# Optimization experiments

Hardware: AMD Instinct MI355X
Metric: run time of the kernel (lower is better)

## Reference

```python
import jax, jax.numpy as jnp
import numpy as np

N, E, C_IN, HID, K, NLAYERS = 1024, 2048, 4, 192, 5, 4


def setup_inputs() -> dict:
    key = jax.random.key(0)
    ks = jax.random.split(key, 24)
    s = 0.05
    x = jax.random.normal(ks[0], (N, C_IN), jnp.float32)
    src = jax.random.randint(ks[1], (E,), 0, N, dtype=jnp.int32)
    off = jax.random.randint(ks[2], (E,), 1, N, dtype=jnp.int32)
    dst = (src + off) % N  # guarantees no self-loops (ChebConv removes them)
    edge_index = jnp.stack([src, dst])  # [2, E] int32
    edge_attr = jax.random.normal(ks[3], (E, C_IN), jnp.float32)
    batch = jnp.zeros((N,), jnp.int32)  # unused by forward, kept for signature fidelity
    inp = {
        'x': x, 'edge_index': edge_index, 'edge_attr': edge_attr, 'batch': batch,
        # ChebConv(4, 192, K=5): K weight mats + bias
        'cheb_w': jax.random.normal(ks[4], (K, C_IN, HID), jnp.float32) * s,
        'cheb_b': jnp.zeros((HID,), jnp.float32),
        # edge encoder Linear(4, 192)
        'eenc_w': jax.random.normal(ks[5], (C_IN, HID), jnp.float32) * s,
        'eenc_b': jnp.zeros((HID,), jnp.float32),
        # 4 NNConv layers, each with MapE2NxN edge MLP (192->192->192*192),
        # root linear (192x192, no bias) and conv bias
        'nn1_w': jax.random.normal(ks[6], (NLAYERS, HID, HID), jnp.float32) * s,
        'nn1_b': jnp.zeros((NLAYERS, HID), jnp.float32),
        'nn2_w': jax.random.normal(ks[7], (NLAYERS, HID, HID * HID), jnp.float32) * (s / 8.0),
        'nn2_b': jnp.zeros((NLAYERS, HID * HID), jnp.float32),
        'root_w': jax.random.normal(ks[8], (NLAYERS, HID, HID), jnp.float32) * s,
        'conv_b': jnp.zeros((NLAYERS, HID), jnp.float32),
        # LayerNorm per DeepGCNLayer
        'ln_g': jnp.ones((NLAYERS, HID), jnp.float32),
        'ln_b': jnp.zeros((NLAYERS, HID), jnp.float32),
        # final Linear(192, 2)
        'out_w': jax.random.normal(ks[9], (HID, 2), jnp.float32) * s,
        'out_b': jnp.zeros((2,), jnp.float32),
    }
    return inp


def _layernorm(v, g, b):
    mu = jnp.mean(v, axis=-1, keepdims=True)
    var = jnp.mean(jnp.square(v - mu), axis=-1, keepdims=True)
    return (v - mu) * jax.lax.rsqrt(var + 1e-5) * g + b


def reference(x, edge_index, edge_attr, batch, cheb_w, cheb_b, eenc_w, eenc_b,
              nn1_w, nn1_b, nn2_w, nn2_b, root_w, conv_b, ln_g, ln_b, out_w, out_b):
    n = x.shape[0]
    src, dst = edge_index[0], edge_index[1]

    # ---- ChebConv (sym norm, lambda_max=2.0) => L_hat = -D^{-1/2} A D^{-1/2} ----
    deg = jax.ops.segment_sum(jnp.ones_like(src, dtype=x.dtype), src, num_segments=n)
    dinv = jnp.where(deg > 0, 1.0 / jnp.sqrt(jnp.maximum(deg, 1.0)), 0.0)
    wnorm = -dinv[src] * dinv[dst]  # [E]

    def lap(v):  # y = L_hat @ v : gather -> weight -> scatter-add
        return jax.ops.segment_sum(wnorm[:, None] * v[src], dst, num_segments=n)

    Tx0 = x
    out = Tx0 @ cheb_w[0]
    Tx1 = lap(Tx0)
    out = out + Tx1 @ cheb_w[1]
    for k in range(2, K):  # Chebyshev recurrence
        Tx2 = 2.0 * lap(Tx1) - Tx0
        out = out + Tx2 @ cheb_w[k]
        Tx0, Tx1 = Tx1, Tx2
    h = out + cheb_b  # [N, HID]

    # ---- edge encoder ----
    ea = edge_attr @ eenc_w + eenc_b  # [E, HID]

    # ---- NNConv: per-edge MLP-generated weight, gather->edge-GEMM->scatter ----
    def nnconv(v, i):
        theta = (ea @ nn1_w[i] + nn1_b[i]) @ nn2_w[i] + nn2_b[i]  # [E, HID*HID]
        theta = theta.reshape(E, HID, HID)
        msg = jnp.einsum('ei,eio->eo', v[src], theta)  # per-edge matvec
        agg = jax.ops.segment_sum(msg, dst, num_segments=n)  # aggr='add'
        return agg + v @ root_w[i] + conv_b[i]

    # layers[0].conv applied directly (no pre-norm/act)
    h = nnconv(h, 0)
    # layers[1:4] are DeepGCNLayer res+: x + conv(dropout(act(norm(x))))
    for i in range(1, NLAYERS):
        z = jax.nn.relu(_layernorm(h, ln_g[i], ln_b[i]))
        h = h + nnconv(z, i)
    # final: act(layers[0].norm(x)), dropout (eval=identity), linear
    h = jax.nn.relu(_layernorm(h, ln_g[0], ln_b[0]))
    return h @ out_w + out_b  # [N, 2]
```

## Files before the change

kernel.cpp:

```cpp
#include <hip/hip_runtime.h>
#include <stdint.h>

typedef _Float16 half8 __attribute__((ext_vector_type(8)));
typedef float f32x4 __attribute__((ext_vector_type(4)));

typedef const __attribute__((address_space(1))) void* gptr_t;
typedef __attribute__((address_space(3))) void* lptr_t;
static __device__ __forceinline__ void gll16(const void* g, void* l) {
  __builtin_amdgcn_global_load_lds((gptr_t)(unsigned long long)g,
                                   (lptr_t)(unsigned int)(unsigned long long)l,
                                   16, 0, 0);
}

__global__ __launch_bounds__(256)
void k_pb(const float* __restrict__ nn2_w, const float* __restrict__ nn2_b,
          const float* __restrict__ eenc_w, const float* __restrict__ eenc_b,
          const float* __restrict__ nn1_w, const float* __restrict__ nn1_b,
          const float* __restrict__ root_w, _Float16* __restrict__ Btl,
          const float* __restrict__ x, const int* __restrict__ ei,
          float* __restrict__ Tx, int* __restrict__ rowptr, int* __restrict__ eord) {
  __shared__ __align__(16) float smem[17344];
  int t = threadIdx.x;
  if (blockIdx.x >= 72) {
    if (blockIdx.x == 72) {
      if (blockIdx.y == 0) {
        float* cur = smem;
        float* yv = smem + 4096;
        float* deg = yv;
        for (int i = t; i < 1024; i += 256) deg[i] = 0.f;
        __syncthreads();
        for (int e = t; e < 2048; e += 256) atomicAdd(&deg[ei[e]], 1.f);
        __syncthreads();
        float wn[8];
#pragma unroll
        for (int i = 0; i < 8; ++i) {
          int e = t + 256 * i;
          int s = ei[e], d = ei[2048 + e];
          float ds = deg[s], dd = deg[d];
          float a = ds > 0.f ? 1.f / sqrtf(fmaxf(ds, 1.f)) : 0.f;
          float bb = dd > 0.f ? 1.f / sqrtf(fmaxf(dd, 1.f)) : 0.f;
          wn[i] = -a * bb;
        }
        __syncthreads();
        float4 prev[4];
#pragma unroll
        for (int q = 0; q < 4; ++q) {
          int i = t + 256 * q;
          float4 xv = ((const float4*)x)[i];
          ((float4*)cur)[i] = xv;
          ((float4*)Tx)[i] = xv;
        }
        __syncthreads();
        for (int rec = 0; rec < 4; ++rec) {
          for (int i = t; i < 4096; i += 256) yv[i] = 0.f;
          __syncthreads();
#pragma unroll
          for (int i = 0; i < 8; ++i) {
            int e = t + 256 * i;
            int s = ei[e], d = ei[2048 + e];
            float wv = wn[i];
#pragma unroll
            for (int c = 0; c < 4; ++c) atomicAdd(&yv[d * 4 + c], wv * cur[s * 4 + c]);
          }
          __syncthreads();
          float a = rec ? 2.f : 1.f;
#pragma unroll
          for (int q = 0; q < 4; ++q) {
            int i = t + 256 * q;
            float4 y4 = ((float4*)yv)[i];
            float4 c4 = ((float4*)cur)[i];
            float4 n4;
            n4.x = a * y4.x - (rec ? prev[q].x : 0.f);
            n4.y = a * y4.y - (rec ? prev[q].y : 0.f);
            n4.z = a * y4.z - (rec ? prev[q].z : 0.f);
            n4.w = a * y4.w - (rec ? prev[q].w : 0.f);
            prev[q] = c4;
            ((float4*)cur)[i] = n4;
            ((float4*)(Tx + (rec + 1) * 4096))[i] = n4;
          }
          __syncthreads();
        }
      } else if (blockIdx.y == 1) {
        int* cnt = (int*)smem;
        int* rp  = (int*)smem + 1024;
        int* wtot = (int*)smem + 2048;
        int lane = t & 63, wv = t >> 6;
        for (int i = t; i < 1024; i += 256) cnt[i] = 0;
        __syncthreads();
        for (int e = t; e < 2048; e += 256) atomicAdd(&cnt[ei[2048 + e]], 1);
        __syncthreads();
        int c0 = cnt[t * 4], c1 = cnt[t * 4 + 1], c2 = cnt[t * 4 + 2], c3 = cnt[t * 4 + 3];
        int s = c0 + c1 + c2 + c3;
        int inc = s;
#pragma unroll
        for (int off = 1; off < 64; off <<= 1) {
          int u = __shfl_up(inc, off);
          if (lane >= off) inc += u;
        }
        if (lane == 63) wtot[wv] = inc;
        __syncthreads();
        int woff = 0;
#pragma unroll
        for (int j = 0; j < 4; ++j) if (j < wv) woff += wtot[j];
        int excl = woff + inc - s;
        int4 r4; r4.x = excl; r4.y = excl + c0; r4.z = excl + c0 + c1; r4.w = excl + c0 + c1 + c2;
        *(int4*)(rowptr + t * 4) = r4;
        if (t == 0) rowptr[1024] = 2048;
        rp[t * 4] = r4.x; rp[t * 4 + 1] = r4.y; rp[t * 4 + 2] = r4.z; rp[t * 4 + 3] = r4.w;
        __syncthreads();
        for (int e = t; e < 2048; e += 256) {
          int d = ei[2048 + e];
          int slot = atomicAdd(&rp[d], 1);
          eord[slot] = e;
        }
      }
      return;
    }
    int l = blockIdx.y;
    for (int idx = t; idx < 36864; idx += 256) {
      float v = root_w[(size_t)l * 36864 + idx];
      int i = idx / 192, o = idx - i * 192;
      Btl[(size_t)l * 221184 + (i >> 3) * 9216 + (size_t)(960 + o) * 8 + (i & 7)] = (_Float16)v;
    }
    return;
  }
  int w = t >> 6, lane = t & 63;
  int l = blockIdx.y;
  int wcol = blockIdx.x * 512 + w * 128;
  const float* W2l = nn2_w + (size_t)l * 7077888;
  char* ldsbase = (char*)smem + w * 16384;
  int rlane = lane >> 5;
  int clane = (lane & 31) << 4;
  float2 nb = *(const float2*)(nn2_b + (size_t)l * 36864 + wcol + 2 * lane);

#define ISSUE(tile)                                                             \
  {                                                                             \
    _Pragma("unroll")                                                           \
    for (int j = 0; j < 4; ++j) {                                               \
      int row = (tile) * 8 + 2 * j + rlane;                                     \
      gll16((const char*)(W2l + (size_t)row * 36864 + wcol) + clane,            \
            ldsbase + ((tile) & 3) * 4096 + j * 1024 + lane * 16);              \
    }                                                                           \
  }

  ISSUE(0); ISSUE(1); ISSUE(2);
  if (t < 192) {
    float a0 = 0.f, a1 = 0.f, a2 = 0.f, a3 = 0.f, a4 = 0.f;
    const float* nw = nn1_w + (size_t)l * 36864 + t;
    for (int k = 0; k < 192; ++k) {
      float nv = nw[(size_t)k * 192];
      a0 += eenc_w[k] * nv;
      a1 += eenc_w[192 + k] * nv;
      a2 += eenc_w[384 + k] * nv;
      a3 += eenc_w[576 + k] * nv;
      a4 += eenc_b[k] * nv;
    }
    smem[16384 + t] = a0; smem[16576 + t] = a1; smem[16768 + t] = a2;
    smem[16960 + t] = a3; smem[17152 + t] = a4 + nn1_b[l * 192 + t];
  }
  __syncthreads();

  float2 a0 = {0.f, 0.f}, a1 = {0.f, 0.f}, a2 = {0.f, 0.f}, a3 = {0.f, 0.f}, a4 = {0.f, 0.f};
  const float* Ms = smem + 16384;
  for (int tile = 0; tile < 24; ++tile) {
    if (tile < 21) ISSUE(tile + 3);
    if (tile < 21)       asm volatile("s_waitcnt vmcnt(12)" ::: "memory");
    else if (tile == 21) asm volatile("s_waitcnt vmcnt(8)" ::: "memory");
    else if (tile == 22) asm volatile("s_waitcnt vmcnt(4)" ::: "memory");
    else                 asm volatile("s_waitcnt vmcnt(0)" ::: "memory");
    const float* wb = smem + w * 4096 + (tile & 3) * 1024;
    const float* Mt = Ms + tile * 8;
#pragma unroll
    for (int r = 0; r < 8; ++r) {
      float2 wv = *(const float2*)(wb + r * 128 + 2 * lane);
      float m0 = Mt[r], m1 = Mt[192 + r], m2 = Mt[384 + r], m3 = Mt[576 + r], m4 = Mt[768 + r];
      a0.x += m0 * wv.x; a0.y += m0 * wv.y;
      a1.x += m1 * wv.x; a1.y += m1 * wv.y;
      a2.x += m2 * wv.x; a2.y += m2 * wv.y;
      a3.x += m3 * wv.x; a3.y += m3 * wv.y;
      a4.x += m4 * wv.x; a4.y += m4 * wv.y;
    }
  }
#undef ISSUE
  a4.x += nb.x; a4.y += nb.y;
  int col = wcol + 2 * lane;
  {
    int i0 = col / 192, o0 = col - i0 * 192;
    _Float16* B0 = Btl + (size_t)l * 221184 + (i0 >> 3) * 9216 + (i0 & 7);
    B0[(size_t)(0 * 192 + o0) * 8] = (_Float16)a0.x;
    B0[(size_t)(1 * 192 + o0) * 8] = (_Float16)a1.x;
    B0[(size_t)(2 * 192 + o0) * 8] = (_Float16)a2.x;
    B0[(size_t)(3 * 192 + o0) * 8] = (_Float16)a3.x;
    B0[(size_t)(4 * 192 + o0) * 8] = (_Float16)a4.x;
    int c1 = col + 1;
    int i1 = c1 / 192, o1 = c1 - i1 * 192;
    _Float16* B1 = Btl + (size_t)l * 221184 + (i1 >> 3) * 9216 + (i1 & 7);
    B1[(size_t)(0 * 192 + o1) * 8] = (_Float16)a0.y;
    B1[(size_t)(1 * 192 + o1) * 8] = (_Float16)a1.y;
    B1[(size_t)(2 * 192 + o1) * 8] = (_Float16)a2.y;
    B1[(size_t)(3 * 192 + o1) * 8] = (_Float16)a3.y;
    B1[(size_t)(4 * 192 + o1) * 8] = (_Float16)a4.y;
  }
}

__global__ __launch_bounds__(256)
void k_y(const _Float16* __restrict__ z16, const _Float16* __restrict__ Btl,
         float* __restrict__ Y, const float* __restrict__ Tx,
         const float* __restrict__ cheb_w, const float* __restrict__ cheb_b, int layer) {
  __shared__ __align__(16) _Float16 Als[12288];
  int t = threadIdx.x;
  int w = t >> 6, lane = t & 63, l15 = lane & 15, q4 = lane >> 4;
  int e0 = blockIdx.x * 64, cb = blockIdx.y;
  if (layer == 0) {
#pragma unroll
    for (int it = 0; it < 6; ++it) {
      int u = it * 256 + t;
      int row = u & 63, ck = u >> 6;
      int n = e0 + row;
      float tv[5][4];
#pragma unroll
      for (int k = 0; k < 5; ++k) {
        float4 t4 = ((const float4*)(Tx + k * 4096))[n];
        tv[k][0] = t4.x; tv[k][1] = t4.y; tv[k][2] = t4.z; tv[k][3] = t4.w;
      }
      union { _Float16 h[8]; uint4 v; } u8;
#pragma unroll
      for (int j = 0; j < 8; ++j) {
        int o = ck * 8 + j;
        float acc = cheb_b[o];
#pragma unroll
        for (int k = 0; k < 5; ++k)
#pragma unroll
          for (int c = 0; c < 4; ++c)
            acc += tv[k][c] * cheb_w[(k * 4 + c) * 192 + o];
        u8.h[j] = (_Float16)acc;
      }
      *(uint4*)(Als + (size_t)u * 8) = u8.v;
    }
    __syncthreads();
  }
  const _Float16* Bt = Btl + (size_t)layer * 221184;
  const _Float16* ap = z16 + (((size_t)q4 * 1024) + e0 + w * 16 + l15) * 8;
  const _Float16* bp = Bt + (((size_t)q4 * 1152) + cb * 192 + l15) * 8;
  f32x4 acc[12] = {};
#pragma unroll
  for (int ks = 0; ks < 6; ++ks) {
    half8 av;
    if (layer == 0)
      av = *(const half8*)(Als + (((size_t)(ks * 4 + q4) * 64) + w * 16 + l15) * 8);
    else
      av = *(const half8*)(ap + (size_t)ks * 4 * 1024 * 8);
#pragma unroll
    for (int nt = 0; nt < 12; ++nt) {
      half8 bv = *(const half8*)(bp + (size_t)ks * 4 * 1152 * 8 + nt * 16 * 8);
      acc[nt] = __builtin_amdgcn_mfma_f32_16x16x32_f16(av, bv, acc[nt], 0, 0, 0);
    }
  }
#pragma unroll
  for (int nt = 0; nt < 12; ++nt) {
    int col = cb * 192 + nt * 16 + l15;
#pragma unroll
    for (int r = 0; r < 4; ++r) {
      int row = e0 + w * 16 + q4 * 4 + r;
      Y[(size_t)row * 1152 + col] = acc[nt][r];
    }
  }
}

__global__ __launch_bounds__(256)
void k_gn(const int* __restrict__ ei, const float* __restrict__ eattr,
          const int* __restrict__ rowptr, const int* __restrict__ eord,
          const float* __restrict__ Y, const float* __restrict__ hp,
          const float* __restrict__ cbv, const float* __restrict__ gg,
          const float* __restrict__ bb, float* __restrict__ ho,
          _Float16* __restrict__ zo, const float* __restrict__ out_w,
          const float* __restrict__ out_b, float* __restrict__ outp, int l) {
  int t = threadIdx.x, w = t >> 6, lane = t & 63;
  int n = blockIdx.x * 4 + w;
  int o0 = lane, o1 = lane + 64, o2 = lane + 128;
  float v0 = 0.f, v1 = 0.f, v2 = 0.f;
  int beg = rowptr[n], end = rowptr[n + 1];
  for (int idx = beg; idx < end; ++idx) {
    int e = eord[idx];
    int s = ei[e];
    float4 u = ((const float4*)eattr)[e];
    const float* yr = Y + (size_t)s * 1152;
    v0 += yr[o0] * u.x + yr[192 + o0] * u.y + yr[384 + o0] * u.z + yr[576 + o0] * u.w + yr[768 + o0];
    v1 += yr[o1] * u.x + yr[192 + o1] * u.y + yr[384 + o1] * u.z + yr[576 + o1] * u.w + yr[768 + o1];
    v2 += yr[o2] * u.x + yr[192 + o2] * u.y + yr[384 + o2] * u.z + yr[576 + o2] * u.w + yr[768 + o2];
  }
  const float* yn = Y + (size_t)n * 1152 + 960;
  v0 += yn[o0] + cbv[o0]; v1 += yn[o1] + cbv[o1]; v2 += yn[o2] + cbv[o2];
  if (l > 0) {
    v0 += hp[n * 192 + o0]; v1 += hp[n * 192 + o1]; v2 += hp[n * 192 + o2];
  }
  if (l < 3) {
    ho[n * 192 + o0] = v0; ho[n * 192 + o1] = v1; ho[n * 192 + o2] = v2;
  }
  float s1 = v0 + v1 + v2, s2 = v0 * v0 + v1 * v1 + v2 * v2;
#pragma unroll
  for (int off = 32; off >= 1; off >>= 1) {
    s1 += __shfl_xor(s1, off);
    s2 += __shfl_xor(s2, off);
  }
  float mu = s1 * (1.f / 192.f);
  float var = s2 * (1.f / 192.f) - mu * mu;
  float rcp = rsqrtf(var + 1e-5f);
  float z0v = fmaxf((v0 - mu) * rcp * gg[o0] + bb[o0], 0.f);
  float z1v = fmaxf((v1 - mu) * rcp * gg[o1] + bb[o1], 0.f);
  float z2v = fmaxf((v2 - mu) * rcp * gg[o2] + bb[o2], 0.f);
  if (l < 3) {
    zo[((size_t)(o0 >> 3) * 1024 + n) * 8 + (o0 & 7)] = (_Float16)z0v;
    zo[((size_t)(o1 >> 3) * 1024 + n) * 8 + (o1 & 7)] = (_Float16)z1v;
    zo[((size_t)(o2 >> 3) * 1024 + n) * 8 + (o2 & 7)] = (_Float16)z2v;
  } else {
    float a0 = z0v * out_w[o0 * 2] + z1v * out_w[o1 * 2] + z2v * out_w[o2 * 2];
    float a1 = z0v * out_w[o0 * 2 + 1] + z1v * out_w[o1 * 2 + 1] + z2v * out_w[o2 * 2 + 1];
#pragma unroll
    for (int off = 32; off >= 1; off >>= 1) {
      a0 += __shfl_xor(a0, off);
      a1 += __shfl_xor(a1, off);
    }
    if (lane == 0) {
      outp[n * 2] = a0 + out_b[0];
      outp[n * 2 + 1] = a1 + out_b[1];
    }
  }
}

extern "C" void kernel_launch(void* const* d_in, const int* in_sizes, int n_in,
                              void* d_out, int out_size, void* d_ws, size_t ws_size,
                              hipStream_t stream) {
  const float* x      = (const float*)d_in[0];
  const int*   ei     = (const int*)  d_in[1];
  const float* eattr  = (const float*)d_in[2];
  const float* cheb_w = (const float*)d_in[4];
  const float* cheb_b = (const float*)d_in[5];
  const float* eenc_w = (const float*)d_in[6];
  const float* eenc_b = (const float*)d_in[7];
  const float* nn1_w  = (const float*)d_in[8];
  const float* nn1_b  = (const float*)d_in[9];
  const float* nn2_w  = (const float*)d_in[10];
  const float* nn2_b  = (const float*)d_in[11];
  const float* root_w = (const float*)d_in[12];
  const float* conv_b = (const float*)d_in[13];
  const float* ln_g   = (const float*)d_in[14];
  const float* ln_bb  = (const float*)d_in[15];
  const float* out_w  = (const float*)d_in[16];
  const float* out_b  = (const float*)d_in[17];
  float* outp = (float*)d_out;
  (void)in_sizes; (void)n_in; (void)out_size; (void)ws_size;

  char* p = (char*)d_ws;
  _Float16* Btl = (_Float16*)p; p += (size_t)4 * 221184 * 2;
  float* Tx     = (float*)p;    p += 5 * 4096 * 4;
  float* Y      = (float*)p;    p += (size_t)1024 * 1152 * 4;
  float* hA     = (float*)p;    p += 196608 * 4;
  float* hB     = (float*)p;    p += 196608 * 4;
  _Float16* zA  = (_Float16*)p; p += 196608 * 2;
  _Float16* zB  = (_Float16*)p; p += 196608 * 2;
  int* rowptr   = (int*)p;      p += 1056 * 4;
  int* eord     = (int*)p;      p += 2048 * 4;

  k_pb<<<dim3(74, 4), 256, 0, stream>>>(nn2_w, nn2_b, eenc_w, eenc_b, nn1_w, nn1_b,
                                        root_w, Btl, x, ei, Tx, rowptr, eord);

  const _Float16* zin[4] = {zA, zA, zB, zA};
  _Float16* zout[4] = {zA, zB, zA, zA};
  float* hout[4] = {hA, hB, hA, hA};
  const float* hres[4] = {hA, hA, hB, hA};
  for (int l = 0; l < 4; ++l) {
    k_y<<<dim3(16, 6), 256, 0, stream>>>(zin[l], Btl, Y, Tx, cheb_w, cheb_b, l);
    k_gn<<<256, 256, 0, stream>>>(ei, eattr, rowptr, eord, Y, hres[l],
                                  conv_b + (size_t)l * 192,
                                  ln_g + (size_t)((l == 3) ? 0 : (l + 1)) * 192,
                                  ln_bb + (size_t)((l == 3) ? 0 : (l + 1)) * 192,
                                  hout[l], zout[l], out_w, out_b, outp, l);
  }
}
```

Before: 287.0 us.

## Reorder NNConv as aggregate-then-GEMM and fuse each layer into one kernel

Each layer now first gathers source-node features scaled by edge attributes per destination node, building a [16 x 1152] A tile in LDS. It then runs one MFMA GEMM against the factored weight, so the per-node Y buffer and the separate gather kernel are no longer needed. The layer-0 Chebyshev projection moves into the setup kernel, and the weight layout changes to match the new row-major tiling. Each layer now uses a single launch of 64 blocks instead of two launches, which cuts Y traffic and launch count but leaves few blocks for parallelism and serialises the Chebyshev projection inside one setup block.

```diff
diff --git a/kernel.cpp b/kernel.cpp
--- a/kernel.cpp
+++ b/kernel.cpp
@@ -18,7 +18,9 @@
           const float* __restrict__ nn1_w, const float* __restrict__ nn1_b,
           const float* __restrict__ root_w, _Float16* __restrict__ Btl,
           const float* __restrict__ x, const int* __restrict__ ei,
-          float* __restrict__ Tx, int* __restrict__ rowptr, int* __restrict__ eord) {
+          float* __restrict__ Tx, int* __restrict__ rowptr, int* __restrict__ eord,
+          const float* __restrict__ cheb_w, const float* __restrict__ cheb_b,
+          _Float16* __restrict__ z0) {
   __shared__ __align__(16) float smem[17344];
   int t = threadIdx.x;
   if (blockIdx.x >= 72) {
@@ -80,6 +82,29 @@
           }
           __syncthreads();
         }
+        for (int n = t; n < 1024; n += 256) {
+          float tv[5][4];
+#pragma unroll
+          for (int k = 0; k < 5; ++k) {
+            float4 t4 = ((const float4*)(Tx + k * 4096))[n];
+            tv[k][0] = t4.x; tv[k][1] = t4.y; tv[k][2] = t4.z; tv[k][3] = t4.w;
+          }
+          for (int ob = 0; ob < 24; ++ob) {
+            union { _Float16 h[8]; uint4 v; } u8;
+#pragma unroll
+            for (int jj = 0; jj < 8; ++jj) {
+              int o = ob * 8 + jj;
+              float acc = cheb_b[o];
+#pragma unroll
+              for (int k = 0; k < 5; ++k)
+#pragma unroll
+                for (int c = 0; c < 4; ++c)
+                  acc += tv[k][c] * cheb_w[(k * 4 + c) * 192 + o];
+              u8.h[jj] = (_Float16)acc;
+            }
+            *(uint4*)(z0 + (size_t)n * 192 + ob * 8) = u8.v;
+          }
+        }
       } else if (blockIdx.y == 1) {
         int* cnt = (int*)smem;
         int* rp  = (int*)smem + 1024;
@@ -118,9 +143,10 @@
     }
     int l = blockIdx.y;
     for (int idx = t; idx < 36864; idx += 256) {
-      float v = root_w[(size_t)l * 36864 + idx];
-      int i = idx / 192, o = idx - i * 192;
-      Btl[(size_t)l * 221184 + (i >> 3) * 9216 + (size_t)(960 + o) * 8 + (i & 7)] = (_Float16)v;
+      float vv = root_w[(size_t)l * 36864 + idx];
+      int k = idx / 192, o = idx - k * 192;
+      int j = 960 + k;
+      Btl[(size_t)l * 221184 + ((size_t)(j >> 3) * 192 + o) * 8 + (j & 7)] = (_Float16)vv;
     }
     return;
   }
@@ -160,7 +186,7 @@
   }
   __syncthreads();
 
-  float2 a0 = {0.f, 0.f}, a1 = {0.f, 0.f}, a2 = {0.f, 0.f}, a3 = {0.f, 0.f}, a4 = {0.f, 0.f};
+  float2 a[5] = {};
   const float* Ms = smem + 16384;
   for (int tile = 0; tile < 24; ++tile) {
     if (tile < 21) ISSUE(tile + 3);
@@ -173,157 +199,161 @@
 #pragma unroll
     for (int r = 0; r < 8; ++r) {
       float2 wv = *(const float2*)(wb + r * 128 + 2 * lane);
-      float m0 = Mt[r], m1 = Mt[192 + r], m2 = Mt[384 + r], m3 = Mt[576 + r], m4 = Mt[768 + r];
-      a0.x += m0 * wv.x; a0.y += m0 * wv.y;
-      a1.x += m1 * wv.x; a1.y += m1 * wv.y;
-      a2.x += m2 * wv.x; a2.y += m2 * wv.y;
-      a3.x += m3 * wv.x; a3.y += m3 * wv.y;
-      a4.x += m4 * wv.x; a4.y += m4 * wv.y;
+#pragma unroll
+      for (int c = 0; c < 5; ++c) {
+        float m = Mt[c * 192 + r];
+        a[c].x += m * wv.x; a[c].y += m * wv.y;
+      }
     }
   }
 #undef ISSUE
-  a4.x += nb.x; a4.y += nb.y;
+  a[4].x += nb.x; a[4].y += nb.y;
   int col = wcol + 2 * lane;
-  {
-    int i0 = col / 192, o0 = col - i0 * 192;
-    _Float16* B0 = Btl + (size_t)l * 221184 + (i0 >> 3) * 9216 + (i0 & 7);
-    B0[(size_t)(0 * 192 + o0) * 8] = (_Float16)a0.x;
-    B0[(size_t)(1 * 192 + o0) * 8] = (_Float16)a1.x;
-    B0[(size_t)(2 * 192 + o0) * 8] = (_Float16)a2.x;
-    B0[(size_t)(3 * 192 + o0) * 8] = (_Float16)a3.x;
-    B0[(size_t)(4 * 192 + o0) * 8] = (_Float16)a4.x;
-    int c1 = col + 1;
-    int i1 = c1 / 192, o1 = c1 - i1 * 192;
-    _Float16* B1 = Btl + (size_t)l * 221184 + (i1 >> 3) * 9216 + (i1 & 7);
-    B1[(size_t)(0 * 192 + o1) * 8] = (_Float16)a0.y;
-    B1[(size_t)(1 * 192 + o1) * 8] = (_Float16)a1.y;
-    B1[(size_t)(2 * 192 + o1) * 8] = (_Float16)a2.y;
-    B1[(size_t)(3 * 192 + o1) * 8] = (_Float16)a3.y;
-    B1[(size_t)(4 * 192 + o1) * 8] = (_Float16)a4.y;
+  _Float16* base = Btl + (size_t)l * 221184;
+#pragma unroll
+  for (int cc = 0; cc < 2; ++cc) {
+    int c0 = col + cc;
+    int i = c0 / 192, o = c0 - i * 192;
+#pragma unroll
+    for (int c = 0; c < 5; ++c) {
+      int j = c * 192 + i;
+      float vv = (cc == 0) ? a[c].x : a[c].y;
+      base[((size_t)(j >> 3) * 192 + o) * 8 + (j & 7)] = (_Float16)vv;
+    }
   }
 }
 
 __global__ __launch_bounds__(256)
-void k_y(const _Float16* __restrict__ z16, const _Float16* __restrict__ Btl,
-         float* __restrict__ Y, const float* __restrict__ Tx,
-         const float* __restrict__ cheb_w, const float* __restrict__ cheb_b, int layer) {
-  __shared__ __align__(16) _Float16 Als[12288];
-  int t = threadIdx.x;
-  int w = t >> 6, lane = t & 63, l15 = lane & 15, q4 = lane >> 4;
-  int e0 = blockIdx.x * 64, cb = blockIdx.y;
-  if (layer == 0) {
-#pragma unroll
-    for (int it = 0; it < 6; ++it) {
-      int u = it * 256 + t;
-      int row = u & 63, ck = u >> 6;
-      int n = e0 + row;
-      float tv[5][4];
-#pragma unroll
-      for (int k = 0; k < 5; ++k) {
-        float4 t4 = ((const float4*)(Tx + k * 4096))[n];
-        tv[k][0] = t4.x; tv[k][1] = t4.y; tv[k][2] = t4.z; tv[k][3] = t4.w;
-      }
-      union { _Float16 h[8]; uint4 v; } u8;
-#pragma unroll
-      for (int j = 0; j < 8; ++j) {
-        int o = ck * 8 + j;
-        float acc = cheb_b[o];
-#pragma unroll
-        for (int k = 0; k < 5; ++k)
-#pragma unroll
-          for (int c = 0; c < 4; ++c)
-            acc += tv[k][c] * cheb_w[(k * 4 + c) * 192 + o];
-        u8.h[j] = (_Float16)acc;
-      }
-      *(uint4*)(Als + (size_t)u * 8) = u8.v;
-    }
+void k_lyr(const _Float16* __restrict__ z16in, const _Float16* __restrict__ B2l,
+           const int* __restrict__ ei, const float4* __restrict__ eattr4,
+           const int* __restrict__ rowptr, const int* __restrict__ eord,
+           const float* __restrict__ hp, const float* __restrict__ cbv,
+           const float* __restrict__ gg, const float* __restrict__ bb,
+           float* __restrict__ ho, _Float16* __restrict__ z16out,
+           const float* __restrict__ out_w, const float* __restrict__ out_b,
+           float* __restrict__ outp, int l) {
+  __shared__ __align__(16) _Float16 A_lds[18432];
+  __shared__ float2 lnred[4][16];
+  __shared__ float2 outred[4][16];
+  int t = threadIdx.x, w = t >> 6, lane = t & 63, l15 = lane & 15, q4 = lane >> 4;
+  int n0 = blockIdx.x * 16;
+  for (int q = 0; q < 4; ++q) {
+    int row = w * 4 + q, n = n0 + row;
+    float g[5][3] = {};
+    int beg = rowptr[n], end = rowptr[n + 1];
+    for (int idx = beg; idx < end; ++idx) {
+      int e = eord[idx];
+      int s = ei[e];
+      float4 u = eattr4[e];
+#pragma unroll
+      for (int m = 0; m < 3; ++m) {
+        float zv = (float)z16in[(size_t)s * 192 + lane + 64 * m];
+        g[0][m] += u.x * zv; g[1][m] += u.y * zv;
+        g[2][m] += u.z * zv; g[3][m] += u.w * zv;
+        g[4][m] += zv;
+      }
+    }
+#pragma unroll
+    for (int m = 0; m < 3; ++m) {
+      int i = lane + 64 * m;
+#pragma unroll
+      for (int c = 0; c < 5; ++c) {
+        int j = c * 192 + i;
+        A_lds[((j >> 3) * 16 + row) * 8 + (j & 7)] = (_Float16)g[c][m];
+      }
+      int j = 960 + i;
+      A_lds[((j >> 3) * 16 + row) * 8 + (j & 7)] = z16in[(size_t)n * 192 + i];
+    }
+  }
+  __syncthreads();
+  f32x4 acc[3] = {};
+  const _Float16* bp = B2l + (((size_t)q4 * 192) + w * 48 + l15) * 8;
+#pragma unroll 4
+  for (int ks = 0; ks < 36; ++ks) {
+    half8 av = *(const half8*)(A_lds + (((ks * 4 + q4) * 16) + l15) * 8);
+#pragma unroll
+    for (int nt = 0; nt < 3; ++nt) {
+      half8 bv = *(const half8*)(bp + ((size_t)ks * 4 * 192 + nt * 16) * 8);
+      acc[nt] = __builtin_amdgcn_mfma_f32_16x16x32_f16(av, bv, acc[nt], 0, 0, 0);
+    }
+  }
+  float v[3][4];
+  float p1[4] = {0.f, 0.f, 0.f, 0.f}, p2[4] = {0.f, 0.f, 0.f, 0.f};
+#pragma unroll
+  for (int r = 0; r < 4; ++r) {
+    int n = n0 + q4 * 4 + r;
+#pragma unroll
+    for (int nt = 0; nt < 3; ++nt) {
+      int col = w * 48 + nt * 16 + l15;
+      float xv = acc[nt][r] + cbv[col];
+      if (l > 0) xv += hp[(size_t)n * 192 + col];
+      if (l < 3) ho[(size_t)n * 192 + col] = xv;
+      v[nt][r] = xv;
+      p1[r] += xv; p2[r] += xv * xv;
+    }
+  }
+#pragma unroll
+  for (int off = 1; off < 16; off <<= 1)
+#pragma unroll
+    for (int r = 0; r < 4; ++r) {
+      p1[r] += __shfl_xor(p1[r], off);
+      p2[r] += __shfl_xor(p2[r], off);
+    }
+  if (l15 == 0)
+#pragma unroll
+    for (int r = 0; r < 4; ++r) lnred[w][q4 * 4 + r] = make_float2(p1[r], p2[r]);
+  __syncthreads();
+  float zvals[3][4];
+#pragma unroll
+  for (int r = 0; r < 4; ++r) {
+    int row = q4 * 4 + r;
+    float s1 = 0.f, s2 = 0.f;
+#pragma unroll
+    for (int ww = 0; ww < 4; ++ww) { float2 pr = lnred[ww][row]; s1 += pr.x; s2 += pr.y; }
+    float mu = s1 * (1.f / 192.f);
+    float var = s2 * (1.f / 192.f) - mu * mu;
+    float rcp = rsqrtf(var + 1e-5f);
+#pragma unroll
+    for (int nt = 0; nt < 3; ++nt) {
+      int col = w * 48 + nt * 16 + l15;
+      zvals[nt][r] = fmaxf((v[nt][r] - mu) * rcp * gg[col] + bb[col], 0.f);
+    }
+  }
+  if (l < 3) {
+#pragma unroll
+    for (int r = 0; r < 4; ++r) {
+      int n = n0 + q4 * 4 + r;
+#pragma unroll
+      for (int nt = 0; nt < 3; ++nt)
+        z16out[(size_t)n * 192 + w * 48 + nt * 16 + l15] = (_Float16)zvals[nt][r];
+    }
+  } else {
+    float po0[4] = {0.f, 0.f, 0.f, 0.f}, po1[4] = {0.f, 0.f, 0.f, 0.f};
+#pragma unroll
+    for (int r = 0; r < 4; ++r)
+#pragma unroll
+      for (int nt = 0; nt < 3; ++nt) {
+        int col = w * 48 + nt * 16 + l15;
+        po0[r] += zvals[nt][r] * out_w[col * 2];
+        po1[r] += zvals[nt][r] * out_w[col * 2 + 1];
+      }
+#pragma unroll
+    for (int off = 1; off < 16; off <<= 1)
+#pragma unroll
+      for (int r = 0; r < 4; ++r) {
+        po0[r] += __shfl_xor(po0[r], off);
+        po1[r] += __shfl_xor(po1[r], off);
+      }
+    if (l15 == 0)
+#pragma unroll
+      for (int r = 0; r < 4; ++r) outred[w][q4 * 4 + r] = make_float2(po0[r], po1[r]);
     __syncthreads();
-  }
-  const _Float16* Bt = Btl + (size_t)layer * 221184;
-  const _Float16* ap = z16 + (((size_t)q4 * 1024) + e0 + w * 16 + l15) * 8;
-  const _Float16* bp = Bt + (((size_t)q4 * 1152) + cb * 192 + l15) * 8;
-  f32x4 acc[12] = {};
-#pragma unroll
-  for (int ks = 0; ks < 6; ++ks) {
-    half8 av;
-    if (layer == 0)
-      av = *(const half8*)(Als + (((size_t)(ks * 4 + q4) * 64) + w * 16 + l15) * 8);
-    else
-      av = *(const half8*)(ap + (size_t)ks * 4 * 1024 * 8);
-#pragma unroll
-    for (int nt = 0; nt < 12; ++nt) {
-      half8 bv = *(const half8*)(bp + (size_t)ks * 4 * 1152 * 8 + nt * 16 * 8);
-      acc[nt] = __builtin_amdgcn_mfma_f32_16x16x32_f16(av, bv, acc[nt], 0, 0, 0);
-    }
-  }
-#pragma unroll
-  for (int nt = 0; nt < 12; ++nt) {
-    int col = cb * 192 + nt * 16 + l15;
-#pragma unroll
-    for (int r = 0; r < 4; ++r) {
-      int row = e0 + w * 16 + q4 * 4 + r;
-      Y[(size_t)row * 1152 + col] = acc[nt][r];
-    }
-  }
-}
-
-__global__ __launch_bounds__(256)
-void k_gn(const int* __restrict__ ei, const float* __restrict__ eattr,
-          const int* __restrict__ rowptr, const int* __restrict__ eord,
-          const float* __restrict__ Y, const float* __restrict__ hp,
-          const float* __restrict__ cbv, const float* __restrict__ gg,
-          const float* __restrict__ bb, float* __restrict__ ho,
-          _Float16* __restrict__ zo, const float* __restrict__ out_w,
-          const float* __restrict__ out_b, float* __restrict__ outp, int l) {
-  int t = threadIdx.x, w = t >> 6, lane = t & 63;
-  int n = blockIdx.x * 4 + w;
-  int o0 = lane, o1 = lane + 64, o2 = lane + 128;
-  float v0 = 0.f, v1 = 0.f, v2 = 0.f;
-  int beg = rowptr[n], end = rowptr[n + 1];
-  for (int idx = beg; idx < end; ++idx) {
-    int e = eord[idx];
-    int s = ei[e];
-    float4 u = ((const float4*)eattr)[e];
-    const float* yr = Y + (size_t)s * 1152;
-    v0 += yr[o0] * u.x + yr[192 + o0] * u.y + yr[384 + o0] * u.z + yr[576 + o0] * u.w + yr[768 + o0];
-    v1 += yr[o1] * u.x + yr[192 + o1] * u.y + yr[384 + o1] * u.z + yr[576 + o1] * u.w + yr[768 + o1];
-    v2 += yr[o2] * u.x + yr[192 + o2] * u.y + yr[384 + o2] * u.z + yr[576 + o2] * u.w + yr[768 + o2];
-  }
-  const float* yn = Y + (size_t)n * 1152 + 960;
-  v0 += yn[o0] + cbv[o0]; v1 += yn[o1] + cbv[o1]; v2 += yn[o2] + cbv[o2];
-  if (l > 0) {
-    v0 += hp[n * 192 + o0]; v1 += hp[n * 192 + o1]; v2 += hp[n * 192 + o2];
-  }
-  if (l < 3) {
-    ho[n * 192 + o0] = v0; ho[n * 192 + o1] = v1; ho[n * 192 + o2] = v2;
-  }
-  float s1 = v0 + v1 + v2, s2 = v0 * v0 + v1 * v1 + v2 * v2;
-#pragma unroll
-  for (int off = 32; off >= 1; off >>= 1) {
-    s1 += __shfl_xor(s1, off);
-    s2 += __shfl_xor(s2, off);
-  }
-  float mu = s1 * (1.f / 192.f);
-  float var = s2 * (1.f / 192.f) - mu * mu;
-  float rcp = rsqrtf(var + 1e-5f);
-  float z0v = fmaxf((v0 - mu) * rcp * gg[o0] + bb[o0], 0.f);
-  float z1v = fmaxf((v1 - mu) * rcp * gg[o1] + bb[o1], 0.f);
-  float z2v = fmaxf((v2 - mu) * rcp * gg[o2] + bb[o2], 0.f);
-  if (l < 3) {
-    zo[((size_t)(o0 >> 3) * 1024 + n) * 8 + (o0 & 7)] = (_Float16)z0v;
-    zo[((size_t)(o1 >> 3) * 1024 + n) * 8 + (o1 & 7)] = (_Float16)z1v;
-    zo[((size_t)(o2 >> 3) * 1024 + n) * 8 + (o2 & 7)] = (_Float16)z2v;
-  } else {
-    float a0 = z0v * out_w[o0 * 2] + z1v * out_w[o1 * 2] + z2v * out_w[o2 * 2];
-    float a1 = z0v * out_w[o0 * 2 + 1] + z1v * out_w[o1 * 2 + 1] + z2v * out_w[o2 * 2 + 1];
-#pragma unroll
-    for (int off = 32; off >= 1; off >>= 1) {
-      a0 += __shfl_xor(a0, off);
-      a1 += __shfl_xor(a1, off);
-    }
-    if (lane == 0) {
-      outp[n * 2] = a0 + out_b[0];
-      outp[n * 2 + 1] = a1 + out_b[1];
+    if (t < 32) {
+      int row = t >> 1, c = t & 1;
+      float s = 0.f;
+#pragma unroll
+      for (int ww = 0; ww < 4; ++ww) { float2 pr = outred[ww][row]; s += (c == 0) ? pr.x : pr.y; }
+      outp[(n0 + row) * 2 + c] = s + out_b[c];
     }
   }
 }
@@ -354,24 +384,25 @@
   char* p = (char*)d_ws;
   _Float16* Btl = (_Float16*)p; p += (size_t)4 * 221184 * 2;
   float* Tx     = (float*)p;    p += 5 * 4096 * 4;
-  float* Y      = (float*)p;    p += (size_t)1024 * 1152 * 4;
   float* hA     = (float*)p;    p += 196608 * 4;
   float* hB     = (float*)p;    p += 196608 * 4;
+  _Float16* z0  = (_Float16*)p; p += 196608 * 2;
   _Float16* zA  = (_Float16*)p; p += 196608 * 2;
   _Float16* zB  = (_Float16*)p; p += 196608 * 2;
   int* rowptr   = (int*)p;      p += 1056 * 4;
   int* eord     = (int*)p;      p += 2048 * 4;
 
   k_pb<<<dim3(74, 4), 256, 0, stream>>>(nn2_w, nn2_b, eenc_w, eenc_b, nn1_w, nn1_b,
-                                        root_w, Btl, x, ei, Tx, rowptr, eord);
-
-  const _Float16* zin[4] = {zA, zA, zB, zA};
+                                        root_w, Btl, x, ei, Tx, rowptr, eord,
+                                        cheb_w, cheb_b, z0);
+
+  const _Float16* zin[4] = {z0, zA, zB, zA};
   _Float16* zout[4] = {zA, zB, zA, zA};
   float* hout[4] = {hA, hB, hA, hA};
   const float* hres[4] = {hA, hA, hB, hA};
   for (int l = 0; l < 4; ++l) {
-    k_y<<<dim3(16, 6), 256, 0, stream>>>(zin[l], Btl, Y, Tx, cheb_w, cheb_b, l);
-    k_gn<<<256, 256, 0, stream>>>(ei, eattr, rowptr, eord, Y, hres[l],
+    k_lyr<<<64, 256, 0, stream>>>(zin[l], Btl + (size_t)l * 221184, ei,
+                                  (const float4*)eattr, rowptr, eord, hres[l],
                                   conv_b + (size_t)l * 192,
                                   ln_g + (size_t)((l == 3) ? 0 : (l + 1)) * 192,
                                   ln_bb + (size_t)((l == 3) ? 0 : (l + 1)) * 192,
```

After: 532.3 us. 85.5% more time.

## Widen nn2 projection tiles per wave and deepen async LDS prefetch pipeline

Applied to the files above, without the earlier changes.

Each wave of the nn2 weight-projection stage now covers 256 columns with float4 loads instead of 128 columns with float2, which halves the block count in that stage. Global-to-LDS tiles are now 4 rows deep with an 8-slot ring and 7 tiles in flight instead of 3. Shared memory roughly doubles, to about 135KB per block. The aim is more bytes in flight per wave to stream the large nn2 weight matrix at higher bandwidth, at the cost of fewer blocks (152 vs 296) across the GPU and lower occupancy.

```diff
diff --git a/kernel.cpp b/kernel.cpp
--- a/kernel.cpp
+++ b/kernel.cpp
@@ -19,10 +19,10 @@
           const float* __restrict__ root_w, _Float16* __restrict__ Btl,
           const float* __restrict__ x, const int* __restrict__ ei,
           float* __restrict__ Tx, int* __restrict__ rowptr, int* __restrict__ eord) {
-  __shared__ __align__(16) float smem[17344];
+  __shared__ __align__(16) float smem[33728];
   int t = threadIdx.x;
-  if (blockIdx.x >= 72) {
-    if (blockIdx.x == 72) {
+  if (blockIdx.x >= 36) {
+    if (blockIdx.x == 36) {
       if (blockIdx.y == 0) {
         float* cur = smem;
         float* yv = smem + 4096;
@@ -126,24 +126,22 @@
   }
   int w = t >> 6, lane = t & 63;
   int l = blockIdx.y;
-  int wcol = blockIdx.x * 512 + w * 128;
+  int wcol = blockIdx.x * 1024 + w * 256;
   const float* W2l = nn2_w + (size_t)l * 7077888;
-  char* ldsbase = (char*)smem + w * 16384;
-  int rlane = lane >> 5;
-  int clane = (lane & 31) << 4;
-  float2 nb = *(const float2*)(nn2_b + (size_t)l * 36864 + wcol + 2 * lane);
+  char* ldsbase = (char*)smem + w * 32768;
+  f32x4 nb4 = *(const f32x4*)(nn2_b + (size_t)l * 36864 + wcol + 4 * lane);
 
 #define ISSUE(tile)                                                             \
   {                                                                             \
     _Pragma("unroll")                                                           \
-    for (int j = 0; j < 4; ++j) {                                               \
-      int row = (tile) * 8 + 2 * j + rlane;                                     \
-      gll16((const char*)(W2l + (size_t)row * 36864 + wcol) + clane,            \
-            ldsbase + ((tile) & 3) * 4096 + j * 1024 + lane * 16);              \
+    for (int r = 0; r < 4; ++r) {                                               \
+      int row = (tile) * 4 + r;                                                 \
+      gll16((const char*)(W2l + (size_t)row * 36864 + wcol) + lane * 16,        \
+            ldsbase + ((tile) & 7) * 4096 + r * 1024 + lane * 16);              \
     }                                                                           \
   }
 
-  ISSUE(0); ISSUE(1); ISSUE(2);
+  ISSUE(0); ISSUE(1); ISSUE(2); ISSUE(3); ISSUE(4); ISSUE(5); ISSUE(6);
   if (t < 192) {
     float a0 = 0.f, a1 = 0.f, a2 = 0.f, a3 = 0.f, a4 = 0.f;
     const float* nw = nn1_w + (size_t)l * 36864 + t;
@@ -155,51 +153,42 @@
       a3 += eenc_w[576 + k] * nv;
       a4 += eenc_b[k] * nv;
     }
-    smem[16384 + t] = a0; smem[16576 + t] = a1; smem[16768 + t] = a2;
-    smem[16960 + t] = a3; smem[17152 + t] = a4 + nn1_b[l * 192 + t];
+    smem[32768 + t] = a0; smem[32960 + t] = a1; smem[33152 + t] = a2;
+    smem[33344 + t] = a3; smem[33536 + t] = a4 + nn1_b[l * 192 + t];
   }
   __syncthreads();
 
-  float2 a0 = {0.f, 0.f}, a1 = {0.f, 0.f}, a2 = {0.f, 0.f}, a3 = {0.f, 0.f}, a4 = {0.f, 0.f};
-  const float* Ms = smem + 16384;
-  for (int tile = 0; tile < 24; ++tile) {
-    if (tile < 21) ISSUE(tile + 3);
-    if (tile < 21)       asm volatile("s_waitcnt vmcnt(12)" ::: "memory");
-    else if (tile == 21) asm volatile("s_waitcnt vmcnt(8)" ::: "memory");
-    else if (tile == 22) asm volatile("s_waitcnt vmcnt(4)" ::: "memory");
+  f32x4 a[5] = {};
+  const float* Ms = smem + 32768;
+  for (int tile = 0; tile < 48; ++tile) {
+    if (tile < 41) ISSUE(tile + 7);
+    if (tile < 41)       asm volatile("s_waitcnt vmcnt(28)" ::: "memory");
+    else if (tile == 41) asm volatile("s_waitcnt vmcnt(24)" ::: "memory");
+    else if (tile == 42) asm volatile("s_waitcnt vmcnt(20)" ::: "memory");
+    else if (tile == 43) asm volatile("s_waitcnt vmcnt(16)" ::: "memory");
+    else if (tile == 44) asm volatile("s_waitcnt vmcnt(12)" ::: "memory");
+    else if (tile == 45) asm volatile("s_waitcnt vmcnt(8)" ::: "memory");
+    else if (tile == 46) asm volatile("s_waitcnt vmcnt(4)" ::: "memory");
     else                 asm volatile("s_waitcnt vmcnt(0)" ::: "memory");
-    const float* wb = smem + w * 4096 + (tile & 3) * 1024;
-    const float* Mt = Ms + tile * 8;
-#pragma unroll
-    for (int r = 0; r < 8; ++r) {
-      float2 wv = *(const float2*)(wb + r * 128 + 2 * lane);
-      float m0 = Mt[r], m1 = Mt[192 + r], m2 = Mt[384 + r], m3 = Mt[576 + r], m4 = Mt[768 + r];
-      a0.x += m0 * wv.x; a0.y += m0 * wv.y;
-      a1.x += m1 * wv.x; a1.y += m1 * wv.y;
-      a2.x += m2 * wv.x; a2.y += m2 * wv.y;
-      a3.x += m3 * wv.x; a3.y += m3 * wv.y;
-      a4.x += m4 * wv.x; a4.y += m4 * wv.y;
+    const float* wb = (const float*)(ldsbase) + (tile & 7) * 1024;
+    const float* Mt = Ms + tile * 4;
+#pragma unroll
+    for (int r = 0; r < 4; ++r) {
+      f32x4 wv = *(const f32x4*)(wb + r * 256 + 4 * lane);
+#pragma unroll
+      for (int c = 0; c < 5; ++c) a[c] += Mt[c * 192 + r] * wv;
     }
   }
 #undef ISSUE
-  a4.x += nb.x; a4.y += nb.y;
-  int col = wcol + 2 * lane;
-  {
-    int i0 = col / 192, o0 = col - i0 * 192;
-    _Float16* B0 = Btl + (size_t)l * 221184 + (i0 >> 3) * 9216 + (i0 & 7);
-    B0[(size_t)(0 * 192 + o0) * 8] = (_Float16)a0.x;
-    B0[(size_t)(1 * 192 + o0) * 8] = (_Float16)a1.x;
-    B0[(size_t)(2 * 192 + o0) * 8] = (_Float16)a2.x;
-    B0[(size_t)(3 * 192 + o0) * 8] = (_Float16)a3.x;
-    B0[(size_t)(4 * 192 + o0) * 8] = (_Float16)a4.x;
-    int c1 = col + 1;
-    int i1 = c1 / 192, o1 = c1 - i1 * 192;
-    _Float16* B1 = Btl + (size_t)l * 221184 + (i1 >> 3) * 9216 + (i1 & 7);
-    B1[(size_t)(0 * 192 + o1) * 8] = (_Float16)a0.y;
-    B1[(size_t)(1 * 192 + o1) * 8] = (_Float16)a1.y;
-    B1[(size_t)(2 * 192 + o1) * 8] = (_Float16)a2.y;
-    B1[(size_t)(3 * 192 + o1) * 8] = (_Float16)a3.y;
-    B1[(size_t)(4 * 192 + o1) * 8] = (_Float16)a4.y;
+  a[4] += nb4;
+#pragma unroll
+  for (int cc = 0; cc < 4; ++cc) {
+    int col = wcol + 4 * lane + cc;
+    int i = col / 192, o = col - i * 192;
+    _Float16* B0 = Btl + (size_t)l * 221184 + (i >> 3) * 9216 + (i & 7);
+#pragma unroll
+    for (int c = 0; c < 5; ++c)
+      B0[(size_t)(c * 192 + o) * 8] = (_Float16)a[c][cc];
   }
 }
 
@@ -362,7 +351,7 @@
   int* rowptr   = (int*)p;      p += 1056 * 4;
   int* eord     = (int*)p;      p += 2048 * 4;
 
-  k_pb<<<dim3(74, 4), 256, 0, stream>>>(nn2_w, nn2_b, eenc_w, eenc_b, nn1_w, nn1_b,
+  k_pb<<<dim3(38, 4), 256, 0, stream>>>(nn2_w, nn2_b, eenc_w, eenc_b, nn1_w, nn1_b,
                                         root_w, Btl, x, ei, Tx, rowptr, eord);
 
   const _Float16* zin[4] = {zA, zA, zB, zA};
```

New measurement: 287.1 us. About the same (+0.0%).
